# Performance work log

Hardware: AMD Instinct MI355X
Metric: run time of the kernel (lower is better)

Reference implementation:

```python
import jax, jax.numpy as jnp
import numpy as np

N, E, IN, H, B, R, ND, K, ER = 50000, 800000, 256, 256, 256, 8, 5000, 16, 20000
LAM = 0.7


def _gat(x, src, dst, W, a_src, a_dst, b):
    """Single-head PyG-style GATConv, add_self_loops=False."""
    h = x @ W                                   # [N,H]
    s = (h @ a_src)[src] + (h @ a_dst)[dst]     # [E]
    e = jax.nn.leaky_relu(s, 0.2)
    m = jax.ops.segment_max(e, dst, num_segments=N)
    m = jnp.where(jnp.isneginf(m), 0.0, m)
    p = jnp.exp(e - m[dst])
    z = jax.ops.segment_sum(p, dst, num_segments=N)
    alpha = p / (z[dst] + 1e-16)                # softmax over incoming edges
    out = jax.ops.segment_sum(alpha[:, None] * h[src], dst, num_segments=N)
    return out + b


def setup_inputs() -> dict:
    key = jax.random.key(0)
    ks = jax.random.split(key, 20)
    d = {}
    d['x'] = jax.random.normal(ks[0], (N, IN), dtype=jnp.float32)
    d['edge_index'] = jax.random.randint(ks[1], (2, E), 0, N)
    d['head_indices'] = jax.random.randint(ks[2], (B,), 0, N)
    d['rel_types'] = jax.random.randint(ks[3], (B,), 0, R)
    d['tail_indices'] = jax.random.randint(ks[4], (B,), 0, N)
    d['g2l'] = jax.random.randint(ks[5], (N,), 0, ND)
    d['rel_edge_src'] = jax.random.randint(ks[6], (3, ER), 0, ND)
    d['sim_neighbors'] = jax.random.randint(ks[7], (ND, K), 0, N)
    d['sim_weights'] = jax.random.uniform(ks[8], (ND, K), dtype=jnp.float32) / K
    sc1 = 1.0 / np.sqrt(IN)
    sc2 = 1.0 / np.sqrt(H)
    d['W1'] = jax.random.normal(ks[9], (IN, H), dtype=jnp.float32) * sc1
    d['a1_src'] = jax.random.normal(ks[10], (H,), dtype=jnp.float32) * sc2
    d['a1_dst'] = jax.random.normal(ks[11], (H,), dtype=jnp.float32) * sc2
    d['b1'] = jnp.zeros((H,), dtype=jnp.float32)
    d['W2'] = jax.random.normal(ks[12], (H, H), dtype=jnp.float32) * sc2
    d['a2_src'] = jax.random.normal(ks[13], (H,), dtype=jnp.float32) * sc2
    d['a2_dst'] = jax.random.normal(ks[14], (H,), dtype=jnp.float32) * sc2
    d['b2'] = jnp.zeros((H,), dtype=jnp.float32)
    d['rel_emb'] = jax.random.normal(ks[15], (R, H), dtype=jnp.float32) * sc2
    return d


def reference(x, edge_index, head_indices, rel_types, tail_indices, g2l,
              rel_edge_src, sim_neighbors, sim_weights,
              W1, a1_src, a1_dst, b1, W2, a2_src, a2_dst, b2, rel_emb):
    src, dst = edge_index[0], edge_index[1]
    # Encoder: GAT -> SiLU -> GAT
    h = _gat(x, src, dst, W1, a1_src, a1_dst, b1)
    h = jax.nn.silu(h)
    node_emb = _gat(h, src, dst, W2, a2_src, a2_dst, b2)  # [N,H]

    # Sequential per-triplet disease-embedding modification (rel 4/5/6)
    def step(emb, tr):
        hi, r = tr
        is_dis = (r >= 4) & (r <= 6)
        ridx = jnp.clip(r - 4, 0, 2)
        local = g2l[hi]
        deg = jnp.sum(rel_edge_src[ridx] == local).astype(emb.dtype)
        c = LAM * jnp.exp(-LAM * deg) + 0.2
        nb = sim_neighbors[local]           # [K]
        w = sim_weights[local]              # [K]
        vec = (w[:, None] * emb[nb]).sum(0)  # weighted neighbor mix
        new = c * vec + (1.0 - c) * emb[hi]
        row = jnp.where(is_dis, new, emb[hi])
        return emb.at[hi].set(row), None

    node_emb, _ = jax.lax.scan(step, node_emb, (head_indices, rel_types))

    # DistMult decode
    head = node_emb[head_indices]
    tail = node_emb[tail_indices]
    rel = rel_emb[rel_types]
    score = (head * rel * tail).sum(-1)
    return jax.nn.sigmoid(score)
```

## Files before the change

kernel.cpp:

```cpp
#include <hip/hip_runtime.h>
#include <cstdint>

#define N_NODES 50000
#define N_EDGES 800000
#define DIM     256
#define BSZ     256
#define ND_     5000
#define KNB     16
#define ER_     20000
#define LAM     0.7f

typedef unsigned int uint;
typedef unsigned short ushort;
typedef __attribute__((ext_vector_type(8))) short bf16x8;
typedef __attribute__((ext_vector_type(4))) float f32x4;

#define MTILES_PAD 3128
#define M_PAD      (MTILES_PAD*16)
#define NB_SCAN    ((N_NODES + 255) / 256)

__device__ __forceinline__ ushort f2bf(float f) {
    uint u = __float_as_uint(f);
    uint r = u + 0x7FFFu + ((u >> 16) & 1u);
    return (ushort)(r >> 16);
}
__device__ __forceinline__ float bf2f(ushort u) {
    return __uint_as_float(((uint)u) << 16);
}


__global__ __launch_bounds__(256)
void pack_a_kernel(const float* __restrict__ A, ushort* __restrict__ out, int M) {
    const int mt = blockIdx.x;
    const int t  = threadIdx.x;
    const int l  = t & 63;
    const int kt0 = (t >> 6) * 2;
    const int row = mt * 16 + (l & 15);
    const int lg  = l >> 4;
#pragma unroll
    for (int p = 0; p < 2; ++p) {
        int kt = kt0 + p;
        float4 v0 = make_float4(0.f, 0.f, 0.f, 0.f);
        float4 v1 = make_float4(0.f, 0.f, 0.f, 0.f);
        if (row < M) {
            v0 = *(const float4*)(A + (size_t)row * 256 + kt * 32 + lg * 4);
            v1 = *(const float4*)(A + (size_t)row * 256 + kt * 32 + lg * 4 + 16);
        }
        ushort us[8];
        us[0] = f2bf(v0.x); us[1] = f2bf(v0.y); us[2] = f2bf(v0.z); us[3] = f2bf(v0.w);
        us[4] = f2bf(v1.x); us[5] = f2bf(v1.y); us[6] = f2bf(v1.z); us[7] = f2bf(v1.w);
        ushort* dst = out + ((size_t)(mt * 8 + kt) * 64 + l) * 8;
        *(uint4*)dst = *(uint4*)us;
    }
}

__global__ __launch_bounds__(256)
void pack_b_kernel(const float* __restrict__ W, ushort* __restrict__ out) {
    const int nt = blockIdx.x;
    const int t  = threadIdx.x;
    const int l  = t & 63;
    const int kt0 = (t >> 6) * 2;
    const int n  = nt * 16 + (l & 15);
    const int lg = l >> 4;
#pragma unroll
    for (int p = 0; p < 2; ++p) {
        int kt = kt0 + p;
        ushort us[8];
#pragma unroll
        for (int j = 0; j < 8; ++j) {
            int kk = (j & 3) + lg * 4 + (j >> 2) * 16;
            us[j] = f2bf(W[(size_t)(kt * 32 + kk) * 256 + n]);
        }
        ushort* dst = out + ((size_t)(nt * 8 + kt) * 64 + l) * 8;
        *(uint4*)dst = *(uint4*)us;
    }
}

__global__ __launch_bounds__(256)
void gemm_bf16_kernel(const ushort* __restrict__ Ap, const ushort* __restrict__ Bp,
                      ushort* __restrict__ H, int M) {
    const int w = threadIdx.x >> 6;
    const int l = threadIdx.x & 63;
    const int mt0 = blockIdx.x * 4;
    f32x4 acc[4][4];
#pragma unroll
    for (int i = 0; i < 4; ++i)
#pragma unroll
        for (int j = 0; j < 4; ++j) acc[i][j] = (f32x4){0.f, 0.f, 0.f, 0.f};

    for (int kt = 0; kt < 8; ++kt) {
        bf16x8 af[4], bfr[4];
#pragma unroll
        for (int mi = 0; mi < 4; ++mi)
            af[mi] = *(const bf16x8*)(Ap + ((size_t)((mt0 + mi) * 8 + kt) * 64 + l) * 8);
#pragma unroll
        for (int ni = 0; ni < 4; ++ni)
            bfr[ni] = *(const bf16x8*)(Bp + ((size_t)((w * 4 + ni) * 8 + kt) * 64 + l) * 8);
#pragma unroll
        for (int mi = 0; mi < 4; ++mi)
#pragma unroll
            for (int ni = 0; ni < 4; ++ni)
                acc[mi][ni] = __builtin_amdgcn_mfma_f32_16x16x32_bf16(
                    af[mi], bfr[ni], acc[mi][ni], 0, 0, 0);
    }
    const int rbase = (l >> 4) * 4;
    const int cb    = (l & 15);
#pragma unroll
    for (int mi = 0; mi < 4; ++mi) {
        int row0 = (mt0 + mi) * 16 + rbase;
#pragma unroll
        for (int r = 0; r < 4; ++r) {
            int row = row0 + r;
            if (row < M) {
#pragma unroll
                for (int ni = 0; ni < 4; ++ni) {
                    int col = (w * 4 + ni) * 16 + cb;
                    H[(size_t)row * 256 + col] = f2bf(acc[mi][ni][r]);
                }
            }
        }
    }
}

__global__ __launch_bounds__(256)
void node_dots_kernel(const ushort* __restrict__ hb,
                      const float* __restrict__ a_src,
                      const float* __restrict__ a_dst,
                      float* __restrict__ hs, float* __restrict__ hd) {
    int node = blockIdx.x * 4 + (threadIdx.x >> 6);
    int lane = threadIdx.x & 63;
    if (node >= N_NODES) return;
    uint2 rv = *(const uint2*)(hb + (size_t)node * DIM + lane * 4);
    float f0 = __uint_as_float(rv.x << 16);
    float f1 = __uint_as_float(rv.x & 0xffff0000u);
    float f2 = __uint_as_float(rv.y << 16);
    float f3 = __uint_as_float(rv.y & 0xffff0000u);
    float4 as = ((const float4*)a_src)[lane];
    float4 ad = ((const float4*)a_dst)[lane];
    float ssum = f0 * as.x + f1 * as.y + f2 * as.z + f3 * as.w;
    float dsum = f0 * ad.x + f1 * ad.y + f2 * ad.z + f3 * ad.w;
#pragma unroll
    for (int off = 32; off; off >>= 1) {
        ssum += __shfl_down(ssum, off);
        dsum += __shfl_down(dsum, off);
    }
    if (lane == 0) { hs[node] = ssum; hd[node] = dsum; }
}

__global__ __launch_bounds__(256)
void hist_kernel(const int* __restrict__ ei, int* __restrict__ deg) {
    int e = blockIdx.x * 256 + threadIdx.x;
    if (e < N_EDGES) atomicAdd(&deg[ei[N_EDGES + e]], 1);
}

__global__ __launch_bounds__(256)
void blockscan_kernel(const int* __restrict__ deg, int* __restrict__ off,
                      int* __restrict__ bsum) {
    __shared__ int s[256];
    const int b = blockIdx.x, t = threadIdx.x;
    const int idx = b * 256 + t;
    int v = (idx < N_NODES) ? deg[idx] : 0;
    s[t] = v;
    __syncthreads();
    for (int o = 1; o < 256; o <<= 1) {
        int x = (t >= o) ? s[t - o] : 0;
        __syncthreads();
        s[t] += x;
        __syncthreads();
    }
    if (idx < N_NODES) off[idx] = s[t] - v;
    if (t == 255) bsum[b] = s[255];
}

__global__ __launch_bounds__(256)
void scan_bsum_kernel(const int* __restrict__ bsum, int* __restrict__ bpre) {
    __shared__ int s[256];
    const int t = threadIdx.x;
    int v = (t < NB_SCAN) ? bsum[t] : 0;
    s[t] = v;
    __syncthreads();
    for (int o = 1; o < 256; o <<= 1) {
        int x = (t >= o) ? s[t - o] : 0;
        __syncthreads();
        s[t] += x;
        __syncthreads();
    }
    if (t < NB_SCAN) bpre[t] = s[t] - v;
    if (t == 255) bpre[NB_SCAN] = s[255];
}

__global__ __launch_bounds__(256)
void add_offsets_kernel(int* __restrict__ off, const int* __restrict__ bpre) {
    const int b = blockIdx.x, t = threadIdx.x;
    const int idx = b * 256 + t;
    if (idx < N_NODES) off[idx] += bpre[b];
    if (b == NB_SCAN - 1 && t == 255) off[N_NODES] = bpre[NB_SCAN];
}

__global__ __launch_bounds__(256)
void scatter_kernel(const int* __restrict__ ei, const int* __restrict__ off,
                    int* __restrict__ cnt, int* __restrict__ csr_src) {
    int e = blockIdx.x * 256 + threadIdx.x;
    if (e >= N_EDGES) return;
    int d = ei[N_EDGES + e];
    int pos = atomicAdd(&cnt[d], 1);
    csr_src[off[d] + pos] = ei[e];
}

__global__ __launch_bounds__(256)
void gat_aggr_kernel(const int* __restrict__ off, const int* __restrict__ csr_src,
                     const float* __restrict__ hs, const float* __restrict__ hd,
                     const ushort* __restrict__ hb, const float* __restrict__ bias,
                     float* __restrict__ outbuf, int do_silu) {
    const int d = blockIdx.x * 4 + (threadIdx.x >> 6);
    const int l = threadIdx.x & 63;
    if (d >= N_NODES) return;
    const int beg = off[d], end = off[d + 1];
    const float hdd = hd[d];

    float acc0 = 0.f, acc1 = 0.f, acc2 = 0.f, acc3 = 0.f;
    float zl = 0.f;

    for (int c0 = beg; c0 < end; c0 += 64) {
        const int cn = min(end - c0, 64);
        int s = 0; float pexp = 0.f;
        if (l < cn) {
            s = csr_src[c0 + l];
            float v = hs[s] + hdd;
            v = (v >= 0.f) ? v : 0.2f * v;
            pexp = __expf(v);
        }
        zl += pexp;
        for (int j = 0; j < cn; ++j) {
            int   sj = __shfl(s, j);
            float pj = __shfl(pexp, j);
            uint2 rv = *(const uint2*)(hb + (size_t)sj * DIM + l * 4);
            acc0 = fmaf(pj, __uint_as_float(rv.x << 16),          acc0);
            acc1 = fmaf(pj, __uint_as_float(rv.x & 0xffff0000u),  acc1);
            acc2 = fmaf(pj, __uint_as_float(rv.y << 16),          acc2);
            acc3 = fmaf(pj, __uint_as_float(rv.y & 0xffff0000u),  acc3);
        }
    }
    float z = zl;
#pragma unroll
    for (int o = 32; o; o >>= 1) z += __shfl_xor(z, o);
    const float inv = (end > beg) ? 1.f / (z + 1e-16f) : 0.f;
    float4 bb = *(const float4*)(bias + l * 4);
    float o0 = acc0 * inv + bb.x;
    float o1 = acc1 * inv + bb.y;
    float o2 = acc2 * inv + bb.z;
    float o3 = acc3 * inv + bb.w;
    if (do_silu) {
        o0 = o0 / (1.f + __expf(-o0));
        o1 = o1 / (1.f + __expf(-o1));
        o2 = o2 / (1.f + __expf(-o2));
        o3 = o3 / (1.f + __expf(-o3));
    }
    *(float4*)(outbuf + (size_t)d * DIM + l * 4) = make_float4(o0, o1, o2, o3);
}

__global__ __launch_bounds__(256)
void deg_c_kernel(const int* __restrict__ rel, const int* __restrict__ head,
                  const int* __restrict__ g2l, const int* __restrict__ res,
                  float* __restrict__ cvals) {
    int b = blockIdx.x;
    int r = rel[b];
    if (r < 4 || r > 6) { if (threadIdx.x == 0) cvals[b] = 0.f; return; }
    int local = g2l[head[b]];
    const int* rr = res + (size_t)(r - 4) * ER_;
    int cnt = 0;
    for (int i = threadIdx.x; i < ER_; i += 256) cnt += (rr[i] == local);
    __shared__ int sdeg;
    if (threadIdx.x == 0) sdeg = 0;
    __syncthreads();
#pragma unroll
    for (int off = 32; off; off >>= 1) cnt += __shfl_down(cnt, off);
    if ((threadIdx.x & 63) == 0) atomicAdd(&sdeg, cnt);
    __syncthreads();
    if (threadIdx.x == 0)
        cvals[b] = LAM * expf(-LAM * (float)sdeg) + 0.2f;
}

__global__ __launch_bounds__(256)
void prep_steps_kernel(const float* __restrict__ emb, const int* __restrict__ head,
                       const int* __restrict__ rel, const int* __restrict__ g2l,
                       const int* __restrict__ nbs, const float* __restrict__ wts,
                       float* __restrict__ vecpre, int* __restrict__ W,
                       int* __restrict__ flags) {
    int b = blockIdx.x;
    int t = threadIdx.x;
    int r = rel[b];
    int dis = (r >= 4 && r <= 6);
    if (t == 0) { flags[b] = 0; W[b] = dis ? head[b] : -1; }
    if (!dis) return;
    int local = g2l[head[b]];
    const int* __restrict__ nb = nbs + (size_t)local * KNB;
    const float* __restrict__ w = wts + (size_t)local * KNB;
    float v0 = 0.f, v1 = 0.f;
#pragma unroll
    for (int k = 0; k < KNB; k += 2) {
        v0 = fmaf(w[k],     emb[(size_t)nb[k] * DIM + t],     v0);
        v1 = fmaf(w[k + 1], emb[(size_t)nb[k + 1] * DIM + t], v1);
    }
    vecpre[(size_t)b * DIM + t] = v0 + v1;
}

__global__ __launch_bounds__(256)
void conflict_kernel(const int* __restrict__ W, const int* __restrict__ head,
                     const int* __restrict__ rel, const int* __restrict__ g2l,
                     const int* __restrict__ nbs, int* __restrict__ flags) {
    int b = blockIdx.x;
    int r = rel[b];
    if (r < 4 || r > 6) return;
    __shared__ int rd[KNB + 1];
    int t = threadIdx.x;
    if (t == 0) rd[KNB] = head[b];
    if (t < KNB) {
        int local = g2l[head[b]];
        rd[t] = nbs[(size_t)local * KNB + t];
    }
    __syncthreads();
    int w = (t != b) ? W[t] : -1;
    if (w >= 0) {
        bool hit = false;
#pragma unroll
        for (int k = 0; k <= KNB; ++k) hit |= (rd[k] == w);
        if (hit) { flags[b] = 1; flags[t] = 1; }
    }
}

__global__ __launch_bounds__(256)
void apply_par_kernel(float* __restrict__ emb, const int* __restrict__ head,
                      const int* __restrict__ rel, const float* __restrict__ cvals,
                      const float* __restrict__ vecpre, const int* __restrict__ flags) {
    int b = blockIdx.x;
    int r = rel[b];
    if (r < 4 || r > 6) return;
    if (flags[b]) return;
    int t = threadIdx.x;
    int hi = head[b];
    float c = cvals[b];
    size_t idx = (size_t)hi * DIM + t;
    emb[idx] = c * vecpre[(size_t)b * DIM + t] + (1.f - c) * emb[idx];
}

__global__ __launch_bounds__(256)
void apply_seq_kernel(float* __restrict__ emb, const int* __restrict__ head,
                      const int* __restrict__ rel, const int* __restrict__ g2l,
                      const int* __restrict__ nbs, const float* __restrict__ wts,
                      const float* __restrict__ cvals, const int* __restrict__ flags) {
    __shared__ int   snb[BSZ][KNB];
    __shared__ float sw[BSZ][KNB];
    __shared__ int   sh[BSZ];
    __shared__ float sc[BSZ];
    __shared__ int   sf[BSZ];
    const int t = threadIdx.x;
    int r = rel[t];
    int dis = (r >= 4 && r <= 6);
    int hi = head[t];
    sh[t] = hi;
    sc[t] = cvals[t];
    sf[t] = dis ? flags[t] : 0;
    if (dis) {
        int local = g2l[hi];
#pragma unroll
        for (int k = 0; k < KNB; ++k) {
            snb[t][k] = nbs[(size_t)local * KNB + k];
            sw[t][k]  = wts[(size_t)local * KNB + k];
        }
    }
    __syncthreads();
    for (int b = 0; b < BSZ; ++b) {
        if (sf[b]) {
            int hh = sh[b];
            float c = sc[b];
            float v0 = 0.f, v1 = 0.f;
#pragma unroll
            for (int k = 0; k < KNB; k += 2) {
                v0 = fmaf(sw[b][k],     emb[(size_t)snb[b][k] * DIM + t],     v0);
                v1 = fmaf(sw[b][k + 1], emb[(size_t)snb[b][k + 1] * DIM + t], v1);
            }
            size_t idx = (size_t)hh * DIM + t;
            emb[idx] = c * (v0 + v1) + (1.f - c) * emb[idx];
        }
    }
}

__global__ __launch_bounds__(256)
void decode_kernel(const float* __restrict__ emb, const int* __restrict__ head,
                   const int* __restrict__ rel, const int* __restrict__ tail,
                   const float* __restrict__ rel_emb, float* __restrict__ out) {
    int b = blockIdx.x, t = threadIdx.x;
    float v = emb[(size_t)head[b] * DIM + t] *
              rel_emb[(size_t)rel[b] * DIM + t] *
              emb[(size_t)tail[b] * DIM + t];
    __shared__ float red[4];
#pragma unroll
    for (int off = 32; off; off >>= 1) v += __shfl_down(v, off);
    int lane = t & 63, w = t >> 6;
    if (lane == 0) red[w] = v;
    __syncthreads();
    if (t == 0) {
        float s = red[0] + red[1] + red[2] + red[3];
        out[b] = 1.f / (1.f + expf(-s));
    }
}

extern "C" void kernel_launch(void* const* d_in, const int* in_sizes, int n_in,
                              void* d_out, int out_size, void* d_ws, size_t ws_size,
                              hipStream_t stream) {
    const float* x        = (const float*)d_in[0];
    const int*   ei       = (const int*)d_in[1];
    const int*   head     = (const int*)d_in[2];
    const int*   rel      = (const int*)d_in[3];
    const int*   tail     = (const int*)d_in[4];
    const int*   g2l      = (const int*)d_in[5];
    const int*   res      = (const int*)d_in[6];
    const int*   nbs      = (const int*)d_in[7];
    const float* wts      = (const float*)d_in[8];
    const float* W1       = (const float*)d_in[9];
    const float* a1s      = (const float*)d_in[10];
    const float* a1d      = (const float*)d_in[11];
    const float* b1       = (const float*)d_in[12];
    const float* W2       = (const float*)d_in[13];
    const float* a2s      = (const float*)d_in[14];
    const float* a2d      = (const float*)d_in[15];
    const float* b2       = (const float*)d_in[16];
    const float* rel_emb  = (const float*)d_in[17];
    float* out = (float*)d_out;

    char* ws = (char*)d_ws;
    size_t off_b = 0;
    auto alloc = [&](size_t bytes) {
        void* pp = ws + off_b;
        off_b += (bytes + 255) & ~(size_t)255;
        return pp;
    };
    float*  bufB    = (float*)alloc((size_t)N_NODES * DIM * 4);
    ushort* hb      = (ushort*)alloc((size_t)N_NODES * DIM * 2);
    float*  hs      = (float*)alloc((size_t)N_NODES * 4);
    float*  hd      = (float*)alloc((size_t)N_NODES * 4);
    int*    deg     = (int*)alloc((size_t)N_NODES * 4);
    int*    offs    = (int*)alloc((size_t)(N_NODES + 1) * 4);
    int*    cnt     = (int*)alloc((size_t)N_NODES * 4);
    int*    csr_src = (int*)alloc((size_t)N_EDGES * 4);
    int*    bsum    = (int*)alloc((size_t)NB_SCAN * 4);
    int*    bpre    = (int*)alloc((size_t)(NB_SCAN + 1) * 4);
    float*  cvals   = (float*)alloc((size_t)BSZ * 4);
    float*  vecpre  = (float*)alloc((size_t)BSZ * DIM * 4);
    int*    Wrows   = (int*)alloc((size_t)BSZ * 4);
    int*    flags   = (int*)alloc((size_t)BSZ * 4);
    ushort* apack   = (ushort*)alloc((size_t)M_PAD * 256 * 2);
    ushort* wpack1  = (ushort*)alloc((size_t)256 * 256 * 2);
    ushort* wpack2  = (ushort*)alloc((size_t)256 * 256 * 2);

    const int edgeBlocks = (N_EDGES + 255) / 256;
    const int gemmBlocks = MTILES_PAD / 4;
    const int nodeBlocks4 = (N_NODES + 3) / 4;

    hipMemsetAsync(deg, 0, (size_t)N_NODES * 4, stream);
    hipMemsetAsync(cnt, 0, (size_t)N_NODES * 4, stream);
    hist_kernel<<<edgeBlocks, 256, 0, stream>>>(ei, deg);
    blockscan_kernel<<<NB_SCAN, 256, 0, stream>>>(deg, offs, bsum);
    scan_bsum_kernel<<<1, 256, 0, stream>>>(bsum, bpre);
    add_offsets_kernel<<<NB_SCAN, 256, 0, stream>>>(offs, bpre);
    scatter_kernel<<<edgeBlocks, 256, 0, stream>>>(ei, offs, cnt, csr_src);
    pack_b_kernel<<<16, 256, 0, stream>>>(W1, wpack1);
    pack_b_kernel<<<16, 256, 0, stream>>>(W2, wpack2);

    pack_a_kernel<<<MTILES_PAD, 256, 0, stream>>>(x, apack, N_NODES);
    gemm_bf16_kernel<<<gemmBlocks, 256, 0, stream>>>(apack, wpack1, hb, N_NODES);
    node_dots_kernel<<<nodeBlocks4, 256, 0, stream>>>(hb, a1s, a1d, hs, hd);
    gat_aggr_kernel<<<nodeBlocks4, 256, 0, stream>>>(offs, csr_src, hs, hd, hb, b1, bufB, 1);

    pack_a_kernel<<<MTILES_PAD, 256, 0, stream>>>(bufB, apack, N_NODES);
    gemm_bf16_kernel<<<gemmBlocks, 256, 0, stream>>>(apack, wpack2, hb, N_NODES);
    node_dots_kernel<<<nodeBlocks4, 256, 0, stream>>>(hb, a2s, a2d, hs, hd);
    gat_aggr_kernel<<<nodeBlocks4, 256, 0, stream>>>(offs, csr_src, hs, hd, hb, b2, bufB, 0);

    deg_c_kernel<<<BSZ, 256, 0, stream>>>(rel, head, g2l, res, cvals);
    prep_steps_kernel<<<BSZ, 256, 0, stream>>>(bufB, head, rel, g2l, nbs, wts,
                                               vecpre, Wrows, flags);
    conflict_kernel<<<BSZ, 256, 0, stream>>>(Wrows, head, rel, g2l, nbs, flags);
    apply_par_kernel<<<BSZ, 256, 0, stream>>>(bufB, head, rel, cvals, vecpre, flags);
    apply_seq_kernel<<<1, 256, 0, stream>>>(bufB, head, rel, g2l, nbs, wts, cvals, flags);
    decode_kernel<<<BSZ, 256, 0, stream>>>(bufB, head, rel, tail, rel_emb, out);
}
```

Measured before the change: 469.8 us.

## Fuse attention dots into GEMM, bf16 layer-1 output, unroll gather, histogram degrees

The per-node attention dot products are now computed in the GEMM epilogue from the fp32 accumulators, which removes the separate node_dots kernel and its re-read of H. The layer-1 GAT output is written as bf16 and repacked by a lighter bf16 pack kernel, halving that intermediate's traffic. The aggregation gather loop is unrolled by four to keep more independent loads in flight. The per-triplet degree scans are replaced by one histogram of the relation edges plus a lookup. The dot products now use unrounded fp32 values rather than bf16 values, which slightly changes numerics.

Result: faster. 427.5 us (-9.0%).

```diff
diff --git a/kernel.cpp b/kernel.cpp
--- a/kernel.cpp
+++ b/kernel.cpp
@@ -24,9 +24,8 @@
     uint r = u + 0x7FFFu + ((u >> 16) & 1u);
     return (ushort)(r >> 16);
 }
-__device__ __forceinline__ float bf2f(ushort u) {
-    return __uint_as_float(((uint)u) << 16);
-}
+__device__ __forceinline__ float bflo(uint u) { return __uint_as_float(u << 16); }
+__device__ __forceinline__ float bfhi(uint u) { return __uint_as_float(u & 0xffff0000u); }
 
 
 __global__ __launch_bounds__(256)
@@ -55,6 +54,27 @@
 }
 
 __global__ __launch_bounds__(256)
+void pack_a_bf16_kernel(const ushort* __restrict__ A, ushort* __restrict__ out, int M) {
+    const int mt = blockIdx.x;
+    const int t  = threadIdx.x;
+    const int l  = t & 63;
+    const int kt0 = (t >> 6) * 2;
+    const int row = mt * 16 + (l & 15);
+    const int lg  = l >> 4;
+#pragma unroll
+    for (int p = 0; p < 2; ++p) {
+        int kt = kt0 + p;
+        uint2 v0 = make_uint2(0u, 0u), v1 = make_uint2(0u, 0u);
+        if (row < M) {
+            v0 = *(const uint2*)(A + (size_t)row * 256 + kt * 32 + lg * 4);
+            v1 = *(const uint2*)(A + (size_t)row * 256 + kt * 32 + 16 + lg * 4);
+        }
+        uint4 o; o.x = v0.x; o.y = v0.y; o.z = v1.x; o.w = v1.y;
+        *(uint4*)(out + ((size_t)(mt * 8 + kt) * 64 + l) * 8) = o;
+    }
+}
+
+__global__ __launch_bounds__(256)
 void pack_b_kernel(const float* __restrict__ W, ushort* __restrict__ out) {
     const int nt = blockIdx.x;
     const int t  = threadIdx.x;
@@ -78,9 +98,14 @@
 
 __global__ __launch_bounds__(256)
 void gemm_bf16_kernel(const ushort* __restrict__ Ap, const ushort* __restrict__ Bp,
-                      ushort* __restrict__ H, int M) {
-    const int w = threadIdx.x >> 6;
-    const int l = threadIdx.x & 63;
+                      ushort* __restrict__ H,
+                      const float* __restrict__ a_src, const float* __restrict__ a_dst,
+                      float* __restrict__ hs, float* __restrict__ hd, int M) {
+    __shared__ float sdS[4][64];
+    __shared__ float sdD[4][64];
+    const int t = threadIdx.x;
+    const int w = t >> 6;
+    const int l = t & 63;
     const int mt0 = blockIdx.x * 4;
     f32x4 acc[4][4];
 #pragma unroll
@@ -105,46 +130,48 @@
     }
     const int rbase = (l >> 4) * 4;
     const int cb    = (l & 15);
+    float asv[4], adv[4];
+#pragma unroll
+    for (int ni = 0; ni < 4; ++ni) {
+        int col = (w * 4 + ni) * 16 + cb;
+        asv[ni] = a_src[col];
+        adv[ni] = a_dst[col];
+    }
 #pragma unroll
     for (int mi = 0; mi < 4; ++mi) {
-        int row0 = (mt0 + mi) * 16 + rbase;
 #pragma unroll
         for (int r = 0; r < 4; ++r) {
-            int row = row0 + r;
-            if (row < M) {
-#pragma unroll
-                for (int ni = 0; ni < 4; ++ni) {
+            int row = (mt0 + mi) * 16 + rbase + r;
+            float ps = 0.f, pd = 0.f;
+#pragma unroll
+            for (int ni = 0; ni < 4; ++ni) {
+                float hv = acc[mi][ni][r];
+                ps = fmaf(hv, asv[ni], ps);
+                pd = fmaf(hv, adv[ni], pd);
+                if (row < M) {
                     int col = (w * 4 + ni) * 16 + cb;
-                    H[(size_t)row * 256 + col] = f2bf(acc[mi][ni][r]);
+                    H[(size_t)row * 256 + col] = f2bf(hv);
                 }
             }
-        }
-    }
-}
-
-__global__ __launch_bounds__(256)
-void node_dots_kernel(const ushort* __restrict__ hb,
-                      const float* __restrict__ a_src,
-                      const float* __restrict__ a_dst,
-                      float* __restrict__ hs, float* __restrict__ hd) {
-    int node = blockIdx.x * 4 + (threadIdx.x >> 6);
-    int lane = threadIdx.x & 63;
-    if (node >= N_NODES) return;
-    uint2 rv = *(const uint2*)(hb + (size_t)node * DIM + lane * 4);
-    float f0 = __uint_as_float(rv.x << 16);
-    float f1 = __uint_as_float(rv.x & 0xffff0000u);
-    float f2 = __uint_as_float(rv.y << 16);
-    float f3 = __uint_as_float(rv.y & 0xffff0000u);
-    float4 as = ((const float4*)a_src)[lane];
-    float4 ad = ((const float4*)a_dst)[lane];
-    float ssum = f0 * as.x + f1 * as.y + f2 * as.z + f3 * as.w;
-    float dsum = f0 * ad.x + f1 * ad.y + f2 * ad.z + f3 * ad.w;
-#pragma unroll
-    for (int off = 32; off; off >>= 1) {
-        ssum += __shfl_down(ssum, off);
-        dsum += __shfl_down(dsum, off);
-    }
-    if (lane == 0) { hs[node] = ssum; hd[node] = dsum; }
+#pragma unroll
+            for (int o = 1; o < 16; o <<= 1) {
+                ps += __shfl_xor(ps, o);
+                pd += __shfl_xor(pd, o);
+            }
+            if (cb == 0) {
+                sdS[w][mi * 16 + rbase + r] = ps;
+                sdD[w][mi * 16 + rbase + r] = pd;
+            }
+        }
+    }
+    __syncthreads();
+    if (t < 64) {
+        int row = mt0 * 16 + t;
+        if (row < M) {
+            hs[row] = sdS[0][t] + sdS[1][t] + sdS[2][t] + sdS[3][t];
+            hd[row] = sdD[0][t] + sdD[1][t] + sdD[2][t] + sdD[3][t];
+        }
+    }
 }
 
 __global__ __launch_bounds__(256)
@@ -211,7 +238,8 @@
 void gat_aggr_kernel(const int* __restrict__ off, const int* __restrict__ csr_src,
                      const float* __restrict__ hs, const float* __restrict__ hd,
                      const ushort* __restrict__ hb, const float* __restrict__ bias,
-                     float* __restrict__ outbuf, int do_silu) {
+                     float* __restrict__ out_f32, ushort* __restrict__ out_bf,
+                     int do_silu) {
     const int d = blockIdx.x * 4 + (threadIdx.x >> 6);
     const int l = threadIdx.x & 63;
     if (d >= N_NODES) return;
@@ -220,6 +248,7 @@
 
     float acc0 = 0.f, acc1 = 0.f, acc2 = 0.f, acc3 = 0.f;
     float zl = 0.f;
+    const ushort* __restrict__ hcol = hb + l * 4;
 
     for (int c0 = beg; c0 < end; c0 += 64) {
         const int cn = min(end - c0, 64);
@@ -231,14 +260,31 @@
             pexp = __expf(v);
         }
         zl += pexp;
-        for (int j = 0; j < cn; ++j) {
+        int j = 0;
+        for (; j + 4 <= cn; j += 4) {
+            int   s0 = __shfl(s, j),     s1 = __shfl(s, j + 1);
+            int   s2 = __shfl(s, j + 2), s3 = __shfl(s, j + 3);
+            float p0 = __shfl(pexp, j),     p1 = __shfl(pexp, j + 1);
+            float p2 = __shfl(pexp, j + 2), p3 = __shfl(pexp, j + 3);
+            uint2 r0 = *(const uint2*)(hcol + (size_t)s0 * DIM);
+            uint2 r1 = *(const uint2*)(hcol + (size_t)s1 * DIM);
+            uint2 r2 = *(const uint2*)(hcol + (size_t)s2 * DIM);
+            uint2 r3 = *(const uint2*)(hcol + (size_t)s3 * DIM);
+            acc0 = fmaf(p0, bflo(r0.x), acc0); acc1 = fmaf(p0, bfhi(r0.x), acc1);
+            acc2 = fmaf(p0, bflo(r0.y), acc2); acc3 = fmaf(p0, bfhi(r0.y), acc3);
+            acc0 = fmaf(p1, bflo(r1.x), acc0); acc1 = fmaf(p1, bfhi(r1.x), acc1);
+            acc2 = fmaf(p1, bflo(r1.y), acc2); acc3 = fmaf(p1, bfhi(r1.y), acc3);
+            acc0 = fmaf(p2, bflo(r2.x), acc0); acc1 = fmaf(p2, bfhi(r2.x), acc1);
+            acc2 = fmaf(p2, bflo(r2.y), acc2); acc3 = fmaf(p2, bfhi(r2.y), acc3);
+            acc0 = fmaf(p3, bflo(r3.x), acc0); acc1 = fmaf(p3, bfhi(r3.x), acc1);
+            acc2 = fmaf(p3, bflo(r3.y), acc2); acc3 = fmaf(p3, bfhi(r3.y), acc3);
+        }
+        for (; j < cn; ++j) {
             int   sj = __shfl(s, j);
             float pj = __shfl(pexp, j);
-            uint2 rv = *(const uint2*)(hb + (size_t)sj * DIM + l * 4);
-            acc0 = fmaf(pj, __uint_as_float(rv.x << 16),          acc0);
-            acc1 = fmaf(pj, __uint_as_float(rv.x & 0xffff0000u),  acc1);
-            acc2 = fmaf(pj, __uint_as_float(rv.y << 16),          acc2);
-            acc3 = fmaf(pj, __uint_as_float(rv.y & 0xffff0000u),  acc3);
+            uint2 rv = *(const uint2*)(hcol + (size_t)sj * DIM);
+            acc0 = fmaf(pj, bflo(rv.x), acc0); acc1 = fmaf(pj, bfhi(rv.x), acc1);
+            acc2 = fmaf(pj, bflo(rv.y), acc2); acc3 = fmaf(pj, bfhi(rv.y), acc3);
         }
     }
     float z = zl;
@@ -256,29 +302,33 @@
         o2 = o2 / (1.f + __expf(-o2));
         o3 = o3 / (1.f + __expf(-o3));
     }
-    *(float4*)(outbuf + (size_t)d * DIM + l * 4) = make_float4(o0, o1, o2, o3);
-}
-
-__global__ __launch_bounds__(256)
-void deg_c_kernel(const int* __restrict__ rel, const int* __restrict__ head,
-                  const int* __restrict__ g2l, const int* __restrict__ res,
+    if (out_bf) {
+        ushort us[4] = {f2bf(o0), f2bf(o1), f2bf(o2), f2bf(o3)};
+        *(uint2*)(out_bf + (size_t)d * DIM + l * 4) = *(uint2*)us;
+    } else {
+        *(float4*)(out_f32 + (size_t)d * DIM + l * 4) = make_float4(o0, o1, o2, o3);
+    }
+}
+
+__global__ __launch_bounds__(256)
+void rel_hist_kernel(const int* __restrict__ res, int* __restrict__ rhist) {
+    int i = blockIdx.x * 256 + threadIdx.x;
+    if (i < 3 * ER_) atomicAdd(&rhist[(i / ER_) * ND_ + res[i]], 1);
+}
+
+__global__ __launch_bounds__(256)
+void cvals_kernel(const int* __restrict__ rel, const int* __restrict__ head,
+                  const int* __restrict__ g2l, const int* __restrict__ rhist,
                   float* __restrict__ cvals) {
-    int b = blockIdx.x;
+    int b = threadIdx.x;
     int r = rel[b];
-    if (r < 4 || r > 6) { if (threadIdx.x == 0) cvals[b] = 0.f; return; }
-    int local = g2l[head[b]];
-    const int* rr = res + (size_t)(r - 4) * ER_;
-    int cnt = 0;
-    for (int i = threadIdx.x; i < ER_; i += 256) cnt += (rr[i] == local);
-    __shared__ int sdeg;
-    if (threadIdx.x == 0) sdeg = 0;
-    __syncthreads();
-#pragma unroll
-    for (int off = 32; off; off >>= 1) cnt += __shfl_down(cnt, off);
-    if ((threadIdx.x & 63) == 0) atomicAdd(&sdeg, cnt);
-    __syncthreads();
-    if (threadIdx.x == 0)
-        cvals[b] = LAM * expf(-LAM * (float)sdeg) + 0.2f;
+    float c = 0.f;
+    if (r >= 4 && r <= 6) {
+        int local = g2l[head[b]];
+        int deg = rhist[(r - 4) * ND_ + local];
+        c = LAM * __expf(-LAM * (float)deg) + 0.2f;
+    }
+    cvals[b] = c;
 }
 
 __global__ __launch_bounds__(256)
@@ -438,6 +488,7 @@
     };
     float*  bufB    = (float*)alloc((size_t)N_NODES * DIM * 4);
     ushort* hb      = (ushort*)alloc((size_t)N_NODES * DIM * 2);
+    ushort* h1b     = (ushort*)alloc((size_t)N_NODES * DIM * 2);
     float*  hs      = (float*)alloc((size_t)N_NODES * 4);
     float*  hd      = (float*)alloc((size_t)N_NODES * 4);
     int*    deg     = (int*)alloc((size_t)N_NODES * 4);
@@ -446,6 +497,7 @@
     int*    csr_src = (int*)alloc((size_t)N_EDGES * 4);
     int*    bsum    = (int*)alloc((size_t)NB_SCAN * 4);
     int*    bpre    = (int*)alloc((size_t)(NB_SCAN + 1) * 4);
+    int*    rhist   = (int*)alloc((size_t)3 * ND_ * 4);
     float*  cvals   = (float*)alloc((size_t)BSZ * 4);
     float*  vecpre  = (float*)alloc((size_t)BSZ * DIM * 4);
     int*    Wrows   = (int*)alloc((size_t)BSZ * 4);
@@ -460,6 +512,7 @@
 
     hipMemsetAsync(deg, 0, (size_t)N_NODES * 4, stream);
     hipMemsetAsync(cnt, 0, (size_t)N_NODES * 4, stream);
+    hipMemsetAsync(rhist, 0, (size_t)3 * ND_ * 4, stream);
     hist_kernel<<<edgeBlocks, 256, 0, stream>>>(ei, deg);
     blockscan_kernel<<<NB_SCAN, 256, 0, stream>>>(deg, offs, bsum);
     scan_bsum_kernel<<<1, 256, 0, stream>>>(bsum, bpre);
@@ -467,18 +520,21 @@
     scatter_kernel<<<edgeBlocks, 256, 0, stream>>>(ei, offs, cnt, csr_src);
     pack_b_kernel<<<16, 256, 0, stream>>>(W1, wpack1);
     pack_b_kernel<<<16, 256, 0, stream>>>(W2, wpack2);
+    rel_hist_kernel<<<(3 * ER_ + 255) / 256, 256, 0, stream>>>(res, rhist);
 
     pack_a_kernel<<<MTILES_PAD, 256, 0, stream>>>(x, apack, N_NODES);
-    gemm_bf16_kernel<<<gemmBlocks, 256, 0, stream>>>(apack, wpack1, hb, N_NODES);
-    node_dots_kernel<<<nodeBlocks4, 256, 0, stream>>>(hb, a1s, a1d, hs, hd);
-    gat_aggr_kernel<<<nodeBlocks4, 256, 0, stream>>>(offs, csr_src, hs, hd, hb, b1, bufB, 1);
-
-    pack_a_kernel<<<MTILES_PAD, 256, 0, stream>>>(bufB, apack, N_NODES);
-    gemm_bf16_kernel<<<gemmBlocks, 256, 0, stream>>>(apack, wpack2, hb, N_NODES);
-    node_dots_kernel<<<nodeBlocks4, 256, 0, stream>>>(hb, a2s, a2d, hs, hd);
-    gat_aggr_kernel<<<nodeBlocks4, 256, 0, stream>>>(offs, csr_src, hs, hd, hb, b2, bufB, 0);
-
-    deg_c_kernel<<<BSZ, 256, 0, stream>>>(rel, head, g2l, res, cvals);
+    gemm_bf16_kernel<<<gemmBlocks, 256, 0, stream>>>(apack, wpack1, hb, a1s, a1d,
+                                                     hs, hd, N_NODES);
+    gat_aggr_kernel<<<nodeBlocks4, 256, 0, stream>>>(offs, csr_src, hs, hd, hb, b1,
+                                                     nullptr, h1b, 1);
+
+    pack_a_bf16_kernel<<<MTILES_PAD, 256, 0, stream>>>(h1b, apack, N_NODES);
+    gemm_bf16_kernel<<<gemmBlocks, 256, 0, stream>>>(apack, wpack2, hb, a2s, a2d,
+                                                     hs, hd, N_NODES);
+    gat_aggr_kernel<<<nodeBlocks4, 256, 0, stream>>>(offs, csr_src, hs, hd, hb, b2,
+                                                     bufB, nullptr, 0);
+
+    cvals_kernel<<<1, 256, 0, stream>>>(rel, head, g2l, rhist, cvals);
     prep_steps_kernel<<<BSZ, 256, 0, stream>>>(bufB, head, rel, g2l, nbs, wts,
                                                vecpre, Wrows, flags);
     conflict_kernel<<<BSZ, 256, 0, stream>>>(Wrows, head, rel, g2l, nbs, flags);
```
